# Kernel tuning notes

Hardware: AMD Instinct MI355X
Metric: run time of the kernel (lower is better)

## Reference

```python
import jax, jax.numpy as jnp
import numpy as np

N_NODES = 100000
N_EDGES = 1600000
D = 128
L = 3


def setup_inputs() -> dict:
    key = jax.random.key(0)
    k1, k2, k3 = jax.random.split(key, 3)
    edge_index = jax.random.randint(k1, (2, N_EDGES), 0, N_NODES, dtype=jnp.int64)
    emb = jax.random.normal(k2, (N_NODES, D), dtype=jnp.float32)
    # Glorot-style scale for the per-layer linear weights
    Ws = jax.random.normal(k3, (L, D, D), dtype=jnp.float32) * (1.0 / np.sqrt(D))
    bs = jnp.zeros((L, D), dtype=jnp.float32)
    return {"edge_index": edge_index, "emb": emb, "Ws": Ws, "bs": bs}


def _gcn_forward(emb, Ws, bs, edge_index):
    n = emb.shape[0]
    self_loop = jnp.arange(n, dtype=edge_index.dtype)
    # PyG GCNConv adds self-loops and uses symmetric normalization
    row = jnp.concatenate([edge_index[0], self_loop])  # source nodes
    col = jnp.concatenate([edge_index[1], self_loop])  # target nodes
    deg = jax.ops.segment_sum(jnp.ones(row.shape[0], dtype=emb.dtype), col, num_segments=n)
    deg_inv_sqrt = jnp.where(deg > 0, jax.lax.rsqrt(jnp.maximum(deg, 1.0)), 0.0)
    norm = deg_inv_sqrt[row] * deg_inv_sqrt[col]  # [E+N]

    x = emb
    for l in range(Ws.shape[0]):
        h = x @ Ws[l]                              # [N, D] linear transform
        msg = h[row] * norm[:, None]               # gather + scale [E+N, D]
        x = jax.ops.segment_sum(msg, col, num_segments=n) + bs[l]  # scatter-add
        x = jax.nn.relu(x)                         # dropout is identity in eval
    return x


def reference(edge_index, emb, Ws, bs) -> jnp.ndarray:
    return _gcn_forward(emb, Ws, bs, edge_index)
```

## Files before the change

kernel.cpp:

```cpp
#include <hip/hip_runtime.h>
#include <hip/hip_fp16.h>
#include <cstdint>
#include <cstddef>

#define N_NODES 100000
#define N_EDGES 1600000
#define D 128
#define NLAYERS 3
#define NB 3125
#define NBLK_E 128
#define EPB 12500
#define ENT_CAP 1024


__global__ __launch_bounds__(512) void hist1_kernel(const int* __restrict__ col,
                                                    int* __restrict__ hmat) {
    __shared__ int hist[NB];
    int b = blockIdx.x, t = threadIdx.x;
    for (int j = t; j < NB; j += 512) hist[j] = 0;
    __syncthreads();
    int base = b * EPB;
    for (int i = t; i < EPB; i += 512) {
        int c = col[base + i];
        atomicAdd(&hist[c >> 5], 1);
    }
    __syncthreads();
    for (int j = t; j < NB; j += 512) hmat[b * NB + j] = hist[j];
}

__global__ void btot_kernel(const int* __restrict__ hmat, int* __restrict__ btot) {
    int j = blockIdx.x * 256 + threadIdx.x;
    if (j < NB) {
        int s = 0;
        for (int b = 0; b < NBLK_E; b++) s += hmat[b * NB + j];
        btot[j] = s;
    }
}

__global__ void bscan_kernel(const int* __restrict__ btot, int* __restrict__ bstart, int nb, int e) {
    __shared__ int lsum[1024];
    int t = threadIdx.x;
    int vals[4];
    int v0 = 0;
#pragma unroll
    for (int j = 0; j < 4; j++) {
        int idx = t * 4 + j;
        int c = (idx < nb) ? btot[idx] : 0;
        vals[j] = c;
        v0 += c;
    }
    lsum[t] = v0;
    __syncthreads();
    for (int off = 1; off < 1024; off <<= 1) {
        int x = (t >= off) ? lsum[t - off] : 0;
        __syncthreads();
        lsum[t] += x;
        __syncthreads();
    }
    int base = lsum[t] - v0;
#pragma unroll
    for (int j = 0; j < 4; j++) {
        int idx = t * 4 + j;
        if (idx < nb) {
            bstart[idx] = base;
            base += vals[j];
        }
    }
    if (t == 0) bstart[nb] = e;
}

__global__ void hoff_kernel(const int* __restrict__ hmat, const int* __restrict__ bstart,
                            int* __restrict__ hoff) {
    int j = blockIdx.x * 256 + threadIdx.x;
    if (j < NB) {
        int run = bstart[j];
        for (int b = 0; b < NBLK_E; b++) {
            hoff[b * NB + j] = run;
            run += hmat[b * NB + j];
        }
    }
}

__global__ __launch_bounds__(512) void scatter_kernel(const int* __restrict__ row,
                                                      const int* __restrict__ col,
                                                      const int* __restrict__ hoff,
                                                      unsigned* __restrict__ bucketbuf) {
    __shared__ int cur[NB];
    int b = blockIdx.x, t = threadIdx.x;
    for (int j = t; j < NB; j += 512) cur[j] = hoff[b * NB + j];
    __syncthreads();
    int base = b * EPB;
    for (int i = t; i < EPB; i += 512) {
        int r = row[base + i], c = col[base + i];
        int pos = atomicAdd(&cur[c >> 5], 1);
        bucketbuf[pos] = ((unsigned)r << 5) | (unsigned)(c & 31);
    }
}

__global__ void fill2_kernel(const unsigned* __restrict__ bucketbuf, const int* __restrict__ bstart,
                             int* __restrict__ offsets, float* __restrict__ dinv,
                             int* __restrict__ src, int n, int e) {
    __shared__ unsigned ent[ENT_CAP];
    __shared__ int hist[32];
    __shared__ int cur[32];
    __shared__ int loff[32];
    int b = blockIdx.x, t = threadIdx.x;
    int s0 = bstart[b];
    int cnt = bstart[b + 1] - s0;
    if (cnt > ENT_CAP) cnt = ENT_CAP;
    if (t < 32) hist[t] = 0;
    __syncthreads();
    for (int i = t; i < cnt; i += 256) {
        unsigned v = bucketbuf[s0 + i];
        ent[i] = v;
        atomicAdd(&hist[v & 31], 1);
    }
    __syncthreads();
    if (t == 0) {
        int run = s0;
#pragma unroll
        for (int j = 0; j < 32; j++) {
            loff[j] = run;
            run += hist[j];
        }
    }
    __syncthreads();
    if (t < 32) {
        int node = b * 32 + t;
        int o = loff[t];
        offsets[node] = o;
        cur[t] = o;
        dinv[node] = rsqrtf((float)(hist[t] + 1));
    }
    if (b == 0 && t == 0) offsets[n] = e;
    __syncthreads();
    for (int i = t; i < cnt; i += 256) {
        unsigned v = ent[i];
        int pos = atomicAdd(&cur[v & 31], 1);
        src[pos] = (int)(v >> 5);
    }
}


__global__ void cast_kernel(const float2* __restrict__ in, __half2* __restrict__ out, int n2) {
    int i = blockIdx.x * 256 + threadIdx.x;
    if (i < n2) {
        float2 v = in[i];
        out[i] = __floats2half2_rn(v.x, v.y);
    }
}

__global__ void agg_kernel(const __half2* __restrict__ xh, const int* __restrict__ offs,
                           const int* __restrict__ src, const float* __restrict__ dinv,
                           float* __restrict__ out) {
    int v = blockIdx.x;
    int f = threadIdx.x;
    float dv = dinv[v];
    float2 xv = __half22float2(xh[(size_t)v * 64 + f]);
    float ax = dv * xv.x;
    float ay = dv * xv.y;
    int i = offs[v], s1 = offs[v + 1];
    for (; i + 3 < s1; i += 4) {
        int sA = src[i], sB = src[i + 1], sC = src[i + 2], sD = src[i + 3];
        float wA = dinv[sA], wB = dinv[sB], wC = dinv[sC], wD = dinv[sD];
        float2 xA = __half22float2(xh[(size_t)sA * 64 + f]);
        float2 xB = __half22float2(xh[(size_t)sB * 64 + f]);
        float2 xC = __half22float2(xh[(size_t)sC * 64 + f]);
        float2 xD = __half22float2(xh[(size_t)sD * 64 + f]);
        ax += xA.x * wA + xB.x * wB + xC.x * wC + xD.x * wD;
        ay += xA.y * wA + xB.y * wB + xC.y * wC + xD.y * wD;
    }
    for (; i < s1; i++) {
        int sA = src[i];
        float wA = dinv[sA];
        float2 xA = __half22float2(xh[(size_t)sA * 64 + f]);
        ax += xA.x * wA;
        ay += xA.y * wA;
    }
    float2 r;
    r.x = dv * ax;
    r.y = dv * ay;
    ((float2*)out)[(size_t)v * 64 + f] = r;
}

__global__ __launch_bounds__(256, 2) void gemm_bias_relu_kernel(
    const float* __restrict__ A, const float* __restrict__ W,
    const float* __restrict__ bias, float* __restrict__ out,
    __half2* __restrict__ xh_out, int write_h) {
    __shared__ float sW[128 * 128];
    __shared__ float sX[32 * 128];
    int t = threadIdx.x;
    int tx = t & 31;
    int ty = t >> 5;
    int row0 = blockIdx.x * 32;

    const float4* W4 = (const float4*)W;
    float4* sW4 = (float4*)sW;
#pragma unroll
    for (int i = 0; i < 16; i++) sW4[t + 256 * i] = W4[t + 256 * i];

    const float4* A4 = (const float4*)A;
    float4* sX4 = (float4*)sX;
#pragma unroll
    for (int i = 0; i < 4; i++) {
        int c = t + 256 * i;
        int r = c >> 5, kc = c & 31;
        sX4[r * 32 + kc] = A4[(size_t)(row0 + r) * 32 + kc];
    }
    __syncthreads();

    float4 acc[4];
#pragma unroll
    for (int r = 0; r < 4; r++) acc[r] = make_float4(0.f, 0.f, 0.f, 0.f);

#define FMA4(a, s, b) a.x += (s) * (b).x; a.y += (s) * (b).y; a.z += (s) * (b).z; a.w += (s) * (b).w;
#pragma unroll 4
    for (int k0 = 0; k0 < 128; k0 += 4) {
        float4 b0 = *(const float4*)&sW[(k0 + 0) * 128 + tx * 4];
        float4 b1 = *(const float4*)&sW[(k0 + 1) * 128 + tx * 4];
        float4 b2 = *(const float4*)&sW[(k0 + 2) * 128 + tx * 4];
        float4 b3 = *(const float4*)&sW[(k0 + 3) * 128 + tx * 4];
#pragma unroll
        for (int r = 0; r < 4; r++) {
            float4 a = *(const float4*)&sX[(ty * 4 + r) * 128 + k0];
            FMA4(acc[r], a.x, b0)
            FMA4(acc[r], a.y, b1)
            FMA4(acc[r], a.z, b2)
            FMA4(acc[r], a.w, b3)
        }
    }
#undef FMA4

    float4 bb = ((const float4*)bias)[tx];
#pragma unroll
    for (int r = 0; r < 4; r++) {
        float4 o;
        o.x = fmaxf(acc[r].x + bb.x, 0.0f);
        o.y = fmaxf(acc[r].y + bb.y, 0.0f);
        o.z = fmaxf(acc[r].z + bb.z, 0.0f);
        o.w = fmaxf(acc[r].w + bb.w, 0.0f);
        size_t rowi = (size_t)(row0 + ty * 4 + r);
        ((float4*)out)[rowi * 32 + tx] = o;
        if (write_h) {
            xh_out[rowi * 64 + tx * 2] = __floats2half2_rn(o.x, o.y);
            xh_out[rowi * 64 + tx * 2 + 1] = __floats2half2_rn(o.z, o.w);
        }
    }
}


extern "C" void kernel_launch(void* const* d_in, const int* in_sizes, int n_in,
                              void* d_out, int out_size, void* d_ws, size_t ws_size,
                              hipStream_t stream) {
    const int* edge = (const int*)d_in[0];
    const float* emb = (const float*)d_in[1];
    const float* Ws = (const float*)d_in[2];
    const float* bs = (const float*)d_in[3];
    float* out = (float*)d_out;

    const int n = N_NODES, e = N_EDGES;
    const int* row = edge;
    const int* col = edge + e;

    char* p = (char*)d_ws;
    float* aggbuf = (float*)p;
    int* hmat = (int*)p;
    int* hoff = hmat + (size_t)NBLK_E * NB;
    p += (size_t)n * D * 4;
    __half2* xh = (__half2*)p;
    unsigned* bucketbuf = (unsigned*)p;
    p += (size_t)n * D * 2;
    int* csr_src  = (int*)p;    p += (size_t)e * 4;
    float* dinv   = (float*)p;  p += (size_t)n * 4;
    int* offsets  = (int*)p;    p += (size_t)(n + 1) * 4;
    int* btot     = (int*)p;    p += (size_t)NB * 4;
    int* bstart   = (int*)p;    p += (size_t)(NB + 1) * 4;

    hist1_kernel<<<NBLK_E, 512, 0, stream>>>(col, hmat);
    btot_kernel<<<(NB + 255) / 256, 256, 0, stream>>>(hmat, btot);
    bscan_kernel<<<1, 1024, 0, stream>>>(btot, bstart, NB, e);
    hoff_kernel<<<(NB + 255) / 256, 256, 0, stream>>>(hmat, bstart, hoff);
    scatter_kernel<<<NBLK_E, 512, 0, stream>>>(row, col, hoff, bucketbuf);
    fill2_kernel<<<NB, 256, 0, stream>>>(bucketbuf, bstart, offsets, dinv, csr_src, n, e);

    int n2 = n * 64;
    cast_kernel<<<(n2 + 255) / 256, 256, 0, stream>>>((const float2*)emb, xh, n2);

    for (int l = 0; l < NLAYERS; l++) {
        agg_kernel<<<n, 64, 0, stream>>>(xh, offsets, csr_src, dinv, aggbuf);
        gemm_bias_relu_kernel<<<n / 32, 256, 0, stream>>>(
            aggbuf, Ws + (size_t)l * D * D, bs + (size_t)l * D, out,
            xh, (l < NLAYERS - 1) ? 1 : 0);
    }
}
```

Before: 549.1 us.

## Pre-scale features by source degree norm and widen aggregation gather unroll

Features stored in half precision are now pre-multiplied by each node's inverse sqrt degree when they are produced (in the cast and GEMM epilogue), so aggregation no longer gathers dinv per neighbor. The aggregation loop is unrolled to 8 outstanding gathers, with a masked tail that replaces the scalar remainder loop. Nontemporal loads and stores are used for the aggregation buffer. The fp32 output is written only on the last layer. Pre-scaling before rounding to half changes rounding slightly. The masked tail issues redundant loads for up to seven padded slots.

```diff
diff --git a/kernel.cpp b/kernel.cpp
--- a/kernel.cpp
+++ b/kernel.cpp
@@ -11,6 +11,9 @@
 #define NBLK_E 128
 #define EPB 12500
 #define ENT_CAP 1024
+
+typedef float f2v __attribute__((ext_vector_type(2)));
+typedef float f4v __attribute__((ext_vector_type(4)));
 
 
 __global__ __launch_bounds__(512) void hist1_kernel(const int* __restrict__ col,
@@ -142,51 +145,70 @@
 }
 
 
-__global__ void cast_kernel(const float2* __restrict__ in, __half2* __restrict__ out, int n2) {
+__global__ void cast_kernel(const float2* __restrict__ in, const float* __restrict__ dinv,
+                            __half2* __restrict__ out, int n2) {
     int i = blockIdx.x * 256 + threadIdx.x;
     if (i < n2) {
+        float d = dinv[i >> 6];
         float2 v = in[i];
-        out[i] = __floats2half2_rn(v.x, v.y);
-    }
-}
-
-__global__ void agg_kernel(const __half2* __restrict__ xh, const int* __restrict__ offs,
-                           const int* __restrict__ src, const float* __restrict__ dinv,
-                           float* __restrict__ out) {
+        out[i] = __floats2half2_rn(d * v.x, d * v.y);
+    }
+}
+
+__global__ void agg_kernel(const __half2* __restrict__ xs, const int* __restrict__ offs,
+                           float* __restrict__ out, const float* __restrict__ dinv,
+                           const int* __restrict__ src) {
     int v = blockIdx.x;
     int f = threadIdx.x;
     float dv = dinv[v];
-    float2 xv = __half22float2(xh[(size_t)v * 64 + f]);
-    float ax = dv * xv.x;
-    float ay = dv * xv.y;
+    float2 a0 = __half22float2(xs[(size_t)v * 64 + f]);
+    float ax = a0.x;
+    float ay = a0.y;
     int i = offs[v], s1 = offs[v + 1];
-    for (; i + 3 < s1; i += 4) {
-        int sA = src[i], sB = src[i + 1], sC = src[i + 2], sD = src[i + 3];
-        float wA = dinv[sA], wB = dinv[sB], wC = dinv[sC], wD = dinv[sD];
-        float2 xA = __half22float2(xh[(size_t)sA * 64 + f]);
-        float2 xB = __half22float2(xh[(size_t)sB * 64 + f]);
-        float2 xC = __half22float2(xh[(size_t)sC * 64 + f]);
-        float2 xD = __half22float2(xh[(size_t)sD * 64 + f]);
-        ax += xA.x * wA + xB.x * wB + xC.x * wC + xD.x * wD;
-        ay += xA.y * wA + xB.y * wB + xC.y * wC + xD.y * wD;
-    }
-    for (; i < s1; i++) {
-        int sA = src[i];
-        float wA = dinv[sA];
-        float2 xA = __half22float2(xh[(size_t)sA * 64 + f]);
-        ax += xA.x * wA;
-        ay += xA.y * wA;
-    }
-    float2 r;
+    for (; i + 7 < s1; i += 8) {
+        int s[8];
+#pragma unroll
+        for (int j = 0; j < 8; j++) s[j] = src[i + j];
+        float2 x[8];
+#pragma unroll
+        for (int j = 0; j < 8; j++) x[j] = __half22float2(xs[(size_t)s[j] * 64 + f]);
+#pragma unroll
+        for (int j = 0; j < 8; j++) {
+            ax += x[j].x;
+            ay += x[j].y;
+        }
+    }
+    if (i < s1) {
+        int last = s1 - 1;
+        int s[8];
+        float m[8];
+#pragma unroll
+        for (int j = 0; j < 8; j++) {
+            int idx = i + j;
+            bool in = idx < s1;
+            s[j] = src[in ? idx : last];
+            m[j] = in ? 1.0f : 0.0f;
+        }
+        float2 x[8];
+#pragma unroll
+        for (int j = 0; j < 8; j++) x[j] = __half22float2(xs[(size_t)s[j] * 64 + f]);
+#pragma unroll
+        for (int j = 0; j < 8; j++) {
+            ax += m[j] * x[j].x;
+            ay += m[j] * x[j].y;
+        }
+    }
+    f2v r;
     r.x = dv * ax;
     r.y = dv * ay;
-    ((float2*)out)[(size_t)v * 64 + f] = r;
+    __builtin_nontemporal_store(r, (f2v*)out + (size_t)v * 64 + f);
 }
 
 __global__ __launch_bounds__(256, 2) void gemm_bias_relu_kernel(
     const float* __restrict__ A, const float* __restrict__ W,
     const float* __restrict__ bias, float* __restrict__ out,
-    __half2* __restrict__ xh_out, int write_h) {
+    __half2* __restrict__ xs_out, const float* __restrict__ dinv,
+    int write_h, int write_out) {
     __shared__ float sW[128 * 128];
     __shared__ float sX[32 * 128];
     int t = threadIdx.x;
@@ -194,18 +216,18 @@
     int ty = t >> 5;
     int row0 = blockIdx.x * 32;
 
-    const float4* W4 = (const float4*)W;
-    float4* sW4 = (float4*)sW;
+    const f4v* W4 = (const f4v*)W;
+    f4v* sW4 = (f4v*)sW;
 #pragma unroll
     for (int i = 0; i < 16; i++) sW4[t + 256 * i] = W4[t + 256 * i];
 
-    const float4* A4 = (const float4*)A;
-    float4* sX4 = (float4*)sX;
+    const f4v* A4 = (const f4v*)A;
+    f4v* sX4 = (f4v*)sX;
 #pragma unroll
     for (int i = 0; i < 4; i++) {
         int c = t + 256 * i;
         int r = c >> 5, kc = c & 31;
-        sX4[r * 32 + kc] = A4[(size_t)(row0 + r) * 32 + kc];
+        sX4[r * 32 + kc] = __builtin_nontemporal_load(&A4[(size_t)(row0 + r) * 32 + kc]);
     }
     __syncthreads();
 
@@ -240,10 +262,15 @@
         o.z = fmaxf(acc[r].z + bb.z, 0.0f);
         o.w = fmaxf(acc[r].w + bb.w, 0.0f);
         size_t rowi = (size_t)(row0 + ty * 4 + r);
-        ((float4*)out)[rowi * 32 + tx] = o;
+        if (write_out) {
+            f4v ov;
+            ov.x = o.x; ov.y = o.y; ov.z = o.z; ov.w = o.w;
+            __builtin_nontemporal_store(ov, (f4v*)out + rowi * 32 + tx);
+        }
         if (write_h) {
-            xh_out[rowi * 64 + tx * 2] = __floats2half2_rn(o.x, o.y);
-            xh_out[rowi * 64 + tx * 2 + 1] = __floats2half2_rn(o.z, o.w);
+            float dr = dinv[rowi];
+            xs_out[rowi * 64 + tx * 2] = __floats2half2_rn(dr * o.x, dr * o.y);
+            xs_out[rowi * 64 + tx * 2 + 1] = __floats2half2_rn(dr * o.z, dr * o.w);
         }
     }
 }
@@ -267,7 +294,7 @@
     int* hmat = (int*)p;
     int* hoff = hmat + (size_t)NBLK_E * NB;
     p += (size_t)n * D * 4;
-    __half2* xh = (__half2*)p;
+    __half2* xs = (__half2*)p;
     unsigned* bucketbuf = (unsigned*)p;
     p += (size_t)n * D * 2;
     int* csr_src  = (int*)p;    p += (size_t)e * 4;
@@ -284,12 +311,13 @@
     fill2_kernel<<<NB, 256, 0, stream>>>(bucketbuf, bstart, offsets, dinv, csr_src, n, e);
 
     int n2 = n * 64;
-    cast_kernel<<<(n2 + 255) / 256, 256, 0, stream>>>((const float2*)emb, xh, n2);
+    cast_kernel<<<(n2 + 255) / 256, 256, 0, stream>>>((const float2*)emb, dinv, xs, n2);
 
     for (int l = 0; l < NLAYERS; l++) {
-        agg_kernel<<<n, 64, 0, stream>>>(xh, offsets, csr_src, dinv, aggbuf);
+        agg_kernel<<<n, 64, 0, stream>>>(xs, offsets, aggbuf, dinv, csr_src);
         gemm_bias_relu_kernel<<<n / 32, 256, 0, stream>>>(
             aggbuf, Ws + (size_t)l * D * D, bs + (size_t)l * D, out,
-            xh, (l < NLAYERS - 1) ? 1 : 0);
-    }
-}
+            xs, dinv,
+            (l < NLAYERS - 1) ? 1 : 0, (l == NLAYERS - 1) ? 1 : 0);
+    }
+}
```

New measurement: 530.1 us. -3.5%, faster.
